# Performance work log

Measured on AMD Instinct MI355X. Metric: run time of the kernel, lower is better.

The kernel has to match this reference:

```python
import jax, jax.numpy as jnp
import numpy as np

B, C, N, D, E = 2048, 3, 1568, 16, 8  # batch, classes, input caps, out dim, in dim
T_ROUTING = 3


def squash(t, axis=-1):
    sq_norm = jnp.sum(t * t, axis=axis, keepdims=True)
    return (sq_norm / (1.0 + sq_norm)) * t / jnp.sqrt(sq_norm)


def setup_inputs() -> dict:
    key = jax.random.key(0)
    k1, k2 = jax.random.split(key)
    x = jax.random.normal(k1, (B, N, E), dtype=jnp.float32)
    W = 0.001 * jax.random.normal(k2, (1, C, N, D, E), dtype=jnp.float32)
    return {"x": x, "W": W}


def reference(x, W):
    # u_hat = W @ x[:, None, :, :, None]  -> (B, C, N, D) (trailing 1-dim dropped)
    u = jnp.einsum('ocnde,bne->bcnd', W, x)
    b = jnp.zeros((B, C, N), dtype=u.dtype)  # routing logits
    v = None
    for _ in range(T_ROUTING):
        c = jax.nn.softmax(b, axis=1)               # coupling coeffs over classes
        s = jnp.einsum('bcnd,bcn->bcd', u, c)       # weighted sum over input caps
        v = squash(s)                               # (B, C, D)
        b = b + jnp.einsum('bcd,bcnd->bcn', v, u)   # agreement update
    return v
```

## Files before the change

### kernel.cpp

```cpp
#include <hip/hip_runtime.h>
#include <hip/hip_fp16.h>

#define BB 2048
#define NN 1568
#define CD 48
#define G  8
#define WSLOTS 98304
#define SFLTS (BB * CD)

typedef _Float16 h2v __attribute__((ext_vector_type(2)));

__device__ __forceinline__ unsigned packh2(float a, float b) {
    __half2 h = __floats2half2_rn(a, b);
    unsigned r; __builtin_memcpy(&r, &h, 4); return r;
}
__device__ __forceinline__ float2 uph2(unsigned v) {
    __half2 h; __builtin_memcpy(&h, &v, 4); return __half22float2(h);
}
__device__ __forceinline__ float fdot2u(unsigned a, unsigned b, float c) {
#if __has_builtin(__builtin_amdgcn_fdot2)
    h2v av, bv;
    __builtin_memcpy(&av, &a, 4); __builtin_memcpy(&bv, &b, 4);
    return __builtin_amdgcn_fdot2(av, bv, c, false);
#else
    const float2 fa = uph2(a), fb = uph2(b);
    return c + fa.x * fb.x + fa.y * fb.y;
#endif
}
__device__ __forceinline__ unsigned hadd2u(unsigned a, unsigned b) {
    __half2 ha, hb; __builtin_memcpy(&ha, &a, 4); __builtin_memcpy(&hb, &b, 4);
    __half2 r = __hadd2(ha, hb);
    unsigned q; __builtin_memcpy(&q, &r, 4); return q;
}
__device__ __forceinline__ unsigned hfma2u(unsigned a, unsigned b, unsigned c) {
    __half2 ha, hb, hc;
    __builtin_memcpy(&ha, &a, 4); __builtin_memcpy(&hb, &b, 4); __builtin_memcpy(&hc, &c, 4);
    __half2 r = __hfma2(ha, hb, hc);
    unsigned q; __builtin_memcpy(&q, &r, 4); return q;
}

__global__ __launch_bounds__(256)
void wcast(const float* __restrict__ W, uint4* __restrict__ Wh)
{
    const int id = blockIdx.x * 256 + threadIdx.x;
    float* sz = (float*)(Wh + WSLOTS);
#pragma unroll
    for (int k = 0; k < 12; ++k) sz[id + k * 24576] = 0.f;

    const int ts = id & 511;
    const int r  = id >> 9;
    const int dq = r & 3;
    const int ci = r >> 2;
    const int g  = ci & 3;
    const int c  = ci >> 2;
    const int n  = g * 512 + ts;
    uint4* dst = Wh + (size_t)ci * 8192 + dq * 4 * 512 + ts;
    if (n < NN) {
        const float* src = W + ((size_t)(c * NN + n)) * 128 + dq * 32;
#pragma unroll
        for (int dd = 0; dd < 4; ++dd) {
            const float4 f0 = *(const float4*)(src + dd * 8);
            const float4 f1 = *(const float4*)(src + dd * 8 + 4);
            uint4 q;
            q.x = packh2(f0.x, f0.y); q.y = packh2(f0.z, f0.w);
            q.z = packh2(f1.x, f1.y); q.w = packh2(f1.z, f1.w);
            dst[dd * 512] = q;
        }
    } else {
        const uint4 z = make_uint4(0u, 0u, 0u, 0u);
#pragma unroll
        for (int dd = 0; dd < 4; ++dd) dst[dd * 512] = z;
    }
}

template<int P>
__global__ __launch_bounds__(512, 1)
void rpass(const float* __restrict__ x, const uint4* __restrict__ Wh,
           const float* __restrict__ s1in, const float* __restrict__ s2in,
           float* __restrict__ sout)
{
    __shared__ uint4 wtile[3072];
    __shared__ unsigned wv2s[G][24];
    const int t    = threadIdx.x;
    const int w    = t >> 6;
    const int lane = t & 63;
    const int chunk = blockIdx.x / (BB / G);
    const int bg    = blockIdx.x % (BB / G);
    const int b     = bg * G + w;

    unsigned wvr[24];
    if (P > 0) {
        if (t < G * CD) {
            const int bl = t / CD, cd = t % CD;
            float v;
            {
                const float a = s1in[(size_t)(bg * G + bl) * CD + cd] * (1.0f / 3.0f);
                float q = a * a;
                q += __shfl_xor(q, 1); q += __shfl_xor(q, 2);
                q += __shfl_xor(q, 4); q += __shfl_xor(q, 8);
                v = a * sqrtf(q) / (1.f + q);
            }
            if (P == 2) {
                const float a = s2in[(size_t)(bg * G + bl) * CD + cd];
                float q = a * a;
                q += __shfl_xor(q, 1); q += __shfl_xor(q, 2);
                q += __shfl_xor(q, 4); q += __shfl_xor(q, 8);
                v += a * sqrtf(q) / (1.f + q);
            }
            const float vn = __shfl_xor(v, 1);
            if ((cd & 1) == 0) wv2s[bl][cd >> 1] = packh2(v, vn);
        }
        __syncthreads();
#pragma unroll
        for (int j = 0; j < 24; ++j) wvr[j] = wv2s[w][j];
    }

    unsigned acc[24];
#pragma unroll
    for (int j = 0; j < 24; ++j) acc[j] = 0u;

    const float* xb = x + (size_t)b * NN * 8;

#define DO_CL(C3, LL) { \
    _Pragma("unroll") \
    for (int dq = 0; dq < 4; ++dq) { \
        const uint4 w0 = wtile[((C3) * 16 + dq * 4 + 0) * 64 + lane]; \
        const uint4 w1 = wtile[((C3) * 16 + dq * 4 + 1) * 64 + lane]; \
        const uint4 w2 = wtile[((C3) * 16 + dq * 4 + 2) * 64 + lane]; \
        const uint4 w3 = wtile[((C3) * 16 + dq * 4 + 3) * 64 + lane]; \
        const float f0 = fdot2u(w0.x,xh0,fdot2u(w0.y,xh1,fdot2u(w0.z,xh2,fdot2u(w0.w,xh3,0.f)))); \
        const float f1 = fdot2u(w1.x,xh0,fdot2u(w1.y,xh1,fdot2u(w1.z,xh2,fdot2u(w1.w,xh3,0.f)))); \
        const float f2 = fdot2u(w2.x,xh0,fdot2u(w2.y,xh1,fdot2u(w2.z,xh2,fdot2u(w2.w,xh3,0.f)))); \
        const float f3 = fdot2u(w3.x,xh0,fdot2u(w3.y,xh1,fdot2u(w3.z,xh2,fdot2u(w3.w,xh3,0.f)))); \
        const unsigned pa = packh2(f0, f1); \
        const unsigned pb = packh2(f2, f3); \
        ur[(C3) * 8 + dq * 2]     = pa; \
        ur[(C3) * 8 + dq * 2 + 1] = pb; \
        if (P > 0) { \
            LL = fdot2u(pa, wvr[(C3) * 8 + dq * 2],     LL); \
            LL = fdot2u(pb, wvr[(C3) * 8 + dq * 2 + 1], LL); \
        } \
    } }

#define DO_CG(C3, LL, GG, TS) { \
    const uint4* wp = Wh + (size_t)((C3) * 4 + (GG)) * 8192 + (TS); \
    _Pragma("unroll") \
    for (int dq = 0; dq < 4; ++dq) { \
        const uint4 w0 = wp[(dq * 4 + 0) * 512]; \
        const uint4 w1 = wp[(dq * 4 + 1) * 512]; \
        const uint4 w2 = wp[(dq * 4 + 2) * 512]; \
        const uint4 w3 = wp[(dq * 4 + 3) * 512]; \
        const float f0 = fdot2u(w0.x,xh0,fdot2u(w0.y,xh1,fdot2u(w0.z,xh2,fdot2u(w0.w,xh3,0.f)))); \
        const float f1 = fdot2u(w1.x,xh0,fdot2u(w1.y,xh1,fdot2u(w1.z,xh2,fdot2u(w1.w,xh3,0.f)))); \
        const float f2 = fdot2u(w2.x,xh0,fdot2u(w2.y,xh1,fdot2u(w2.z,xh2,fdot2u(w2.w,xh3,0.f)))); \
        const float f3 = fdot2u(w3.x,xh0,fdot2u(w3.y,xh1,fdot2u(w3.z,xh2,fdot2u(w3.w,xh3,0.f)))); \
        const unsigned pa = packh2(f0, f1); \
        const unsigned pb = packh2(f2, f3); \
        ur[(C3) * 8 + dq * 2]     = pa; \
        ur[(C3) * 8 + dq * 2 + 1] = pb; \
        if (P > 0) { \
            LL = fdot2u(pa, wvr[(C3) * 8 + dq * 2],     LL); \
            LL = fdot2u(pb, wvr[(C3) * 8 + dq * 2 + 1], LL); \
        } \
    } }

#define ROW_TAIL(BODY0, BODY1, BODY2, NROW) { \
    const float4 xa = __ldg((const float4*)(xb + (size_t)(NROW) * 8)); \
    const float4 xc = __ldg((const float4*)(xb + (size_t)(NROW) * 8 + 4)); \
    const unsigned xh0 = packh2(xa.x, xa.y), xh1 = packh2(xa.z, xa.w); \
    const unsigned xh2 = packh2(xc.x, xc.y), xh3 = packh2(xc.z, xc.w); \
    unsigned ur[24]; \
    float l0 = 0.f, l1 = 0.f, l2 = 0.f; \
    BODY0 BODY1 BODY2 \
    if (P == 0) { \
        (void)l0; (void)l1; (void)l2; \
        _Pragma("unroll") for (int j = 0; j < 24; ++j) acc[j] = hadd2u(acc[j], ur[j]); \
    } else { \
        const float e0 = __expf(l0), e1 = __expf(l1), e2 = __expf(l2); \
        const float inv = 1.f / (e0 + e1 + e2); \
        const unsigned c0h = packh2(e0 * inv, e0 * inv); \
        const unsigned c1h = packh2(e1 * inv, e1 * inv); \
        const unsigned c2h = packh2(e2 * inv, e2 * inv); \
        _Pragma("unroll") for (int j = 0; j < 8; ++j) { \
            acc[j]      = hfma2u(c0h, ur[j],      acc[j]); \
            acc[8 + j]  = hfma2u(c1h, ur[8 + j],  acc[8 + j]); \
            acc[16 + j] = hfma2u(c2h, ur[16 + j], acc[16 + j]); \
        } \
    } }

#pragma unroll 1
    for (int r = 0; r < 8; ++r) {
#pragma unroll
        for (int k = 0; k < 6; ++k) {
            const int q  = t + k * 512;
            const int s  = q >> 6;
            const int to = q & 63;
            wtile[q] = Wh[(size_t)((s >> 4) * 4 + chunk) * 8192 + (s & 15) * 512 + r * 64 + to];
        }
        __syncthreads();
        {
            const int n = chunk * 512 + r * 64 + lane;
            ROW_TAIL(DO_CL(0, l0), DO_CL(1, l1), DO_CL(2, l2), n)
        }
        __syncthreads();
    }
    if (chunk == 2 && lane < 32) {
        const int n = 1536 + lane;
        ROW_TAIL(DO_CG(0, l0, 3, lane), DO_CG(1, l1, 3, lane), DO_CG(2, l2, 3, lane), n)
    }
#undef ROW_TAIL
#undef DO_CG
#undef DO_CL

    float myv = 0.f;
#pragma unroll
    for (int j = 0; j < 24; ++j) {
        float2 g_ = uph2(acc[j]);
        g_.x += __shfl_xor(g_.x, 1);  g_.y += __shfl_xor(g_.y, 1);
        g_.x += __shfl_xor(g_.x, 2);  g_.y += __shfl_xor(g_.y, 2);
        g_.x += __shfl_xor(g_.x, 4);  g_.y += __shfl_xor(g_.y, 4);
        g_.x += __shfl_xor(g_.x, 8);  g_.y += __shfl_xor(g_.y, 8);
        g_.x += __shfl_xor(g_.x, 16); g_.y += __shfl_xor(g_.y, 16);
        g_.x += __shfl_xor(g_.x, 32); g_.y += __shfl_xor(g_.y, 32);
        if ((lane >> 1) == j) myv = (lane & 1) ? g_.y : g_.x;
    }
    if (lane < CD) atomicAdd(&sout[(size_t)b * CD + lane], myv);
}

__global__ __launch_bounds__(256)
void fsquash(const float* __restrict__ s3, float* __restrict__ out)
{
    const int idx = blockIdx.x * 256 + threadIdx.x;
    const float s = s3[idx];
    float q = s * s;
    q += __shfl_xor(q, 1); q += __shfl_xor(q, 2);
    q += __shfl_xor(q, 4); q += __shfl_xor(q, 8);
    out[idx] = s * sqrtf(q) / (1.f + q);
}

extern "C" void kernel_launch(void* const* d_in, const int* in_sizes, int n_in,
                              void* d_out, int out_size, void* d_ws, size_t ws_size,
                              hipStream_t stream) {
    (void)in_sizes; (void)n_in; (void)out_size;
    const float* x = (const float*)d_in[0];
    const float* W = (const float*)d_in[1];
    if (ws_size < (size_t)WSLOTS * 16 + (size_t)3 * SFLTS * 4) return;
    uint4* Wh = (uint4*)d_ws;
    float* s1 = (float*)d_ws + (size_t)WSLOTS * 4;
    float* s2 = s1 + SFLTS;
    float* s3 = s2 + SFLTS;

    hipLaunchKernelGGL(wcast,    dim3(96),           dim3(256), 0, stream, W, Wh);
    hipLaunchKernelGGL(rpass<0>, dim3(3 * (BB / G)), dim3(512), 0, stream, x, Wh, s1, s2, s1);
    hipLaunchKernelGGL(rpass<1>, dim3(3 * (BB / G)), dim3(512), 0, stream, x, Wh, s1, s2, s2);
    hipLaunchKernelGGL(rpass<2>, dim3(3 * (BB / G)), dim3(512), 0, stream, x, Wh, s1, s2, s3);
    hipLaunchKernelGGL(fsquash,  dim3(384),          dim3(256), 0, stream, s3, (float*)d_out);
}
```

Baseline: 441.9 us.

## Software-pipeline W tile and x loads into registers ahead of compute

Prefetches the next row's W tile slices and x values into registers before computing the current row, then writes them to shared memory after compute. Global load latency is meant to overlap with the fdot2 compute instead of stalling at the top of each iteration. The cost is extra live registers (six uint4 plus two float4) in a kernel that is already register-heavy, which may reduce occupancy. It also precomputes the W gather offsets once outside the loop.

Measured after the change: 1.252 ms. 183% more time.

```diff
diff --git a/kernel.cpp b/kernel.cpp
--- a/kernel.cpp
+++ b/kernel.cpp
@@ -121,6 +121,30 @@
 
     const float* xb = x + (size_t)b * NN * 8;
 
+#define GBASE(K) g##K
+    int g0, g1, g2, g3, g4, g5;
+    {
+#define MKB(K) { const int q = t + (K) * 512; const int s = q >> 6; \
+                 GBASE(K) = ((s >> 4) * 4 + chunk) * 8192 + (s & 15) * 512 + (q & 63); }
+        MKB(0) MKB(1) MKB(2) MKB(3) MKB(4) MKB(5)
+#undef MKB
+    }
+    const int nb = chunk * 512 + lane;
+
+    uint4 p0, p1, p2, p3, p4, p5;
+    float4 xpa, xpc;
+#define ISSUE_W(R) { p0 = Wh[g0 + (R) * 64]; p1 = Wh[g1 + (R) * 64]; \
+                     p2 = Wh[g2 + (R) * 64]; p3 = Wh[g3 + (R) * 64]; \
+                     p4 = Wh[g4 + (R) * 64]; p5 = Wh[g5 + (R) * 64]; }
+#define ISSUE_X(R) { const float* xp_ = xb + (size_t)(nb + (R) * 64) * 8; \
+                     xpa = *(const float4*)xp_; xpc = *(const float4*)(xp_ + 4); }
+#define WRITE_W()  { wtile[t] = p0; wtile[t + 512] = p1; wtile[t + 1024] = p2; \
+                     wtile[t + 1536] = p3; wtile[t + 2048] = p4; wtile[t + 2560] = p5; }
+
+    ISSUE_W(0) ISSUE_X(0)
+    WRITE_W()
+    __syncthreads();
+
 #define DO_CL(C3, LL) { \
     _Pragma("unroll") \
     for (int dq = 0; dq < 4; ++dq) { \
@@ -164,11 +188,9 @@
         } \
     } }
 
-#define ROW_TAIL(BODY0, BODY1, BODY2, NROW) { \
-    const float4 xa = __ldg((const float4*)(xb + (size_t)(NROW) * 8)); \
-    const float4 xc = __ldg((const float4*)(xb + (size_t)(NROW) * 8 + 4)); \
-    const unsigned xh0 = packh2(xa.x, xa.y), xh1 = packh2(xa.z, xa.w); \
-    const unsigned xh2 = packh2(xc.x, xc.y), xh3 = packh2(xc.z, xc.w); \
+#define ROW_TAIL(BODY0, BODY1, BODY2, XA, XC) { \
+    const unsigned xh0 = packh2((XA).x, (XA).y), xh1 = packh2((XA).z, (XA).w); \
+    const unsigned xh2 = packh2((XC).x, (XC).y), xh3 = packh2((XC).z, (XC).w); \
     unsigned ur[24]; \
     float l0 = 0.f, l1 = 0.f, l2 = 0.f; \
     BODY0 BODY1 BODY2 \
@@ -190,27 +212,28 @@
 
 #pragma unroll 1
     for (int r = 0; r < 8; ++r) {
-#pragma unroll
-        for (int k = 0; k < 6; ++k) {
-            const int q  = t + k * 512;
-            const int s  = q >> 6;
-            const int to = q & 63;
-            wtile[q] = Wh[(size_t)((s >> 4) * 4 + chunk) * 8192 + (s & 15) * 512 + r * 64 + to];
+        const float4 xa = xpa, xc = xpc;
+        if (r < 7) { ISSUE_W(r + 1) ISSUE_X(r + 1) }
+        ROW_TAIL(DO_CL(0, l0), DO_CL(1, l1), DO_CL(2, l2), xa, xc)
+        if (r < 7) {
+            __syncthreads();
+            WRITE_W()
+            __syncthreads();
         }
-        __syncthreads();
-        {
-            const int n = chunk * 512 + r * 64 + lane;
-            ROW_TAIL(DO_CL(0, l0), DO_CL(1, l1), DO_CL(2, l2), n)
-        }
-        __syncthreads();
     }
     if (chunk == 2 && lane < 32) {
         const int n = 1536 + lane;
-        ROW_TAIL(DO_CG(0, l0, 3, lane), DO_CG(1, l1, 3, lane), DO_CG(2, l2, 3, lane), n)
+        const float4 xa = *(const float4*)(xb + (size_t)n * 8);
+        const float4 xc = *(const float4*)(xb + (size_t)n * 8 + 4);
+        ROW_TAIL(DO_CG(0, l0, 3, lane), DO_CG(1, l1, 3, lane), DO_CG(2, l2, 3, lane), xa, xc)
     }
 #undef ROW_TAIL
 #undef DO_CG
 #undef DO_CL
+#undef ISSUE_W
+#undef ISSUE_X
+#undef WRITE_W
+#undef GBASE
 
     float myv = 0.f;
 #pragma unroll
```
